# Performance work log

Hardware: AMD Instinct MI355X
Metric: run time of the kernel (lower is better)

Reference implementation:

```python
import jax, jax.numpy as jnp
import numpy as np

B, L, D = 1, 2048, 768
H, DH = 12, 64  # n_heads, d_head (D // H)
LN_EPS = 1e-5
DEN_EPS = 1e-6


def setup_inputs() -> dict:
    key = jax.random.key(0)
    ks = jax.random.split(key, 11)
    s = 0.02
    return {
        "x": jax.random.normal(ks[0], (B, L, D), dtype=jnp.float32),
        "W_qkv": jax.random.normal(ks[1], (D, 3 * D), dtype=jnp.float32) * s,
        "b_qkv": jnp.zeros((3 * D,), dtype=jnp.float32),
        "W_sem": jax.random.normal(ks[2], (D, 2 * D), dtype=jnp.float32) * s,
        "b_sem": jnp.zeros((2 * D,), dtype=jnp.float32),
        "W_ctx": jax.random.normal(ks[3], (D, 2 * D), dtype=jnp.float32) * s,
        "b_ctx": jnp.zeros((2 * D,), dtype=jnp.float32),
        "W_proj": jax.random.normal(ks[4], (D, D), dtype=jnp.float32) * s,
        "b_proj": jnp.zeros((D,), dtype=jnp.float32),
        "ln_g": jnp.ones((D,), dtype=jnp.float32),
        "ln_b": jnp.zeros((D,), dtype=jnp.float32),
    }


def _heads(t):
    # [B,L,D] -> [B,H,L,DH]
    return t.reshape(B, L, H, DH).transpose(0, 2, 1, 3)


def reference(x, W_qkv, b_qkv, W_sem, b_sem, W_ctx, b_ctx, W_proj, b_proj, ln_g, ln_b):
    # LayerNorm
    mu = jnp.mean(x, axis=-1, keepdims=True)
    var = jnp.mean(jnp.square(x - mu), axis=-1, keepdims=True)
    x_norm = (x - mu) * jax.lax.rsqrt(var + LN_EPS) * ln_g + ln_b

    qkv = x_norm @ W_qkv + b_qkv
    q, k, v = jnp.split(qkv, 3, axis=-1)

    # interference gate from raw x
    sem = x @ W_sem + b_sem
    sem_amp = jax.nn.softplus(sem[..., :D])
    sem_phase = sem[..., D:]
    ctx = x @ W_ctx + b_ctx
    ctx_amp = jax.nn.softplus(ctx[..., :D])
    ctx_phase = ctx[..., D:]
    gate = jax.nn.sigmoid(sem_amp * ctx_amp * jnp.cos(sem_phase - ctx_phase))
    k = k * gate

    q_f = jax.nn.elu(_heads(q)) + 1.0  # [B,H,L,DH]
    k_f = jax.nn.elu(_heads(k)) + 1.0
    v_f = _heads(v)

    # causal linear attention: cumsum of kv outer products along L
    kv = jnp.einsum("bhld,bhle->bhlde", k_f, v_f)  # [B,H,L,DH,DH]
    kv_cum = jnp.cumsum(kv, axis=2)
    out_num = jnp.einsum("bhld,bhlde->bhle", q_f, kv_cum)  # [B,H,L,DH]

    k_cum = jnp.cumsum(k_f, axis=2)
    out_den = jnp.sum(q_f * k_cum, axis=-1, keepdims=True) + DEN_EPS

    attn = (out_num / out_den).transpose(0, 2, 1, 3).reshape(B, L, D)
    return attn @ W_proj + b_proj
```

## Files before the change

kernel.cpp:

```cpp
#include <hip/hip_runtime.h>
#include <math.h>

#define LSEQ 2048
#define DMODEL 768
#define NHEAD 12
#define DHEAD 64
#define NCHUNK 32
#define NMERGED 5376

typedef unsigned short ushort_t;
typedef __attribute__((ext_vector_type(8))) short short8;
typedef float float4v __attribute__((ext_vector_type(4)));

__device__ __forceinline__ ushort_t f2b(float f) {
    union { float f; unsigned int u; } v; v.f = f;
    unsigned int u = v.u;
    return (ushort_t)((u + 0x7fffu + ((u >> 16) & 1u)) >> 16);
}
__device__ __forceinline__ float b2f(ushort_t u) {
    union { unsigned int u; float f; } v; v.u = ((unsigned int)u) << 16;
    return v.f;
}

__device__ __forceinline__ void gl_lds16(const ushort_t* g, ushort_t* l) {
    __builtin_amdgcn_global_load_lds(
        (const __attribute__((address_space(1))) unsigned int*)g,
        (__attribute__((address_space(3))) unsigned int*)l, 16, 0, 0);
}

__global__ void pre_kernel(const float* __restrict__ x, const float* __restrict__ g,
                           const float* __restrict__ beta, ushort_t* __restrict__ xn,
                           ushort_t* __restrict__ xb,
                           const float* __restrict__ Wq, const float* __restrict__ Ws,
                           const float* __restrict__ Wc, ushort_t* __restrict__ Tm,
                           const float* __restrict__ Wp, ushort_t* __restrict__ Tp) {
    __shared__ float red[4];
    __shared__ float bc;
    __shared__ float tile[32][33];
    int tid = threadIdx.x;
    if (blockIdx.x < 2048) {
        int row = blockIdx.x;
        const float* xr = x + (size_t)row * DMODEL;
        float v0 = xr[tid], v1 = xr[tid + 256], v2 = xr[tid + 512];
        float s = v0 + v1 + v2;
#pragma unroll
        for (int o = 32; o > 0; o >>= 1) s += __shfl_down(s, o);
        if ((tid & 63) == 0) red[tid >> 6] = s;
        __syncthreads();
        if (tid == 0) bc = (red[0] + red[1] + red[2] + red[3]) * (1.0f / DMODEL);
        __syncthreads();
        float mu = bc;
        float d0 = v0 - mu, d1 = v1 - mu, d2 = v2 - mu;
        float vs = d0 * d0 + d1 * d1 + d2 * d2;
        __syncthreads();
#pragma unroll
        for (int o = 32; o > 0; o >>= 1) vs += __shfl_down(vs, o);
        if ((tid & 63) == 0) red[tid >> 6] = vs;
        __syncthreads();
        if (tid == 0) bc = rsqrtf((red[0] + red[1] + red[2] + red[3]) * (1.0f / DMODEL) + 1e-5f);
        __syncthreads();
        float r = bc;
        ushort_t* xo = xn + (size_t)row * DMODEL;
        ushort_t* xc = xb + (size_t)row * DMODEL;
        xo[tid]       = f2b(d0 * r * g[tid]       + beta[tid]);
        xo[tid + 256] = f2b(d1 * r * g[tid + 256] + beta[tid + 256]);
        xo[tid + 512] = f2b(d2 * r * g[tid + 512] + beta[tid + 512]);
        xc[tid]       = f2b(v0);
        xc[tid + 256] = f2b(v1);
        xc[tid + 512] = f2b(v2);
    } else {
        int bid = blockIdx.x - 2048;
        int nb = bid % 72;
        int kb = (bid / 72) % 24;
        int zb = bid / (72 * 24);
        const float* W; ushort_t* Wt; int N;
        switch (zb) {
            case 0: W = Wq; Wt = Tm;                        N = 2304; break;
            case 1: W = Ws; Wt = Tm + (size_t)2304 * 768;   N = 1536; break;
            case 2: W = Wc; Wt = Tm + (size_t)3840 * 768;   N = 1536; break;
            default: W = Wp; Wt = Tp;                       N = 768;  break;
        }
        int nbase = nb * 32;
        if (nbase >= N) return;
        int tr = tid >> 5, tc = tid & 31;
        int kbase = kb * 32;
#pragma unroll
        for (int p = 0; p < 4; p++) {
            int r = p * 8 + tr;
            tile[r][tc] = W[(size_t)(kbase + r) * N + nbase + tc];
        }
        __syncthreads();
#pragma unroll
        for (int p = 0; p < 4; p++) {
            int r = p * 8 + tr;
            Wt[(size_t)(nbase + r) * 768 + kbase + tc] = f2b(tile[tc][r]);
        }
    }
}

__global__ __launch_bounds__(256) void gemm_merged_kernel(
    const ushort_t* __restrict__ Axn, const ushort_t* __restrict__ Axb,
    const ushort_t* __restrict__ Bt,
    const float* __restrict__ b_qkv, const float* __restrict__ b_sem,
    const float* __restrict__ b_ctx, ushort_t* __restrict__ Cb,
    ushort_t* __restrict__ vb) {
    const int K = 768;
    __shared__ ushort_t As[128 * 32];
    __shared__ ushort_t Bs[128 * 32];
    int tid = threadIdx.x;
    int wave = tid >> 6, lane = tid & 63;
    int wm = (wave >> 1) * 64, wn = (wave & 1) * 64;
    int quad = lane >> 4, l16 = lane & 15;
    int bid = blockIdx.x;
    int xcd = bid & 7, slot = bid >> 3;
    int tile_id = xcd * 84 + slot;
    int m0 = (tile_id & 15) * 128;
    int n0 = (tile_id >> 4) * 128;
    const ushort_t* A = (n0 < 2304) ? Axn : Axb;
    const float* bias = (n0 < 2304) ? (b_qkv + n0) : (n0 < 3840 ? (b_sem + n0 - 2304) : (b_ctx + n0 - 3840));

    int r0 = tid >> 2;
    int kc = (tid & 3) * 8;
    const ushort_t* Ag0 = A + (size_t)(m0 + r0) * K + kc;
    const ushort_t* Ag1 = A + (size_t)(m0 + 64 + r0) * K + kc;
    const ushort_t* Bg0 = Bt + (size_t)(n0 + r0) * K + kc;
    const ushort_t* Bg1 = Bt + (size_t)(n0 + 64 + r0) * K + kc;
    ushort_t* Al0 = &As[(wave * 64) * 8];
    ushort_t* Al1 = &As[(256 + wave * 64) * 8];
    ushort_t* Bl0 = &Bs[(wave * 64) * 8];
    ushort_t* Bl1 = &Bs[(256 + wave * 64) * 8];

    float4v acc[4][4];
#pragma unroll
    for (int i = 0; i < 4; i++)
#pragma unroll
        for (int j = 0; j < 4; j++)
#pragma unroll
            for (int r = 0; r < 4; r++) acc[i][j][r] = 0.0f;

    for (int k0 = 0; k0 < K; k0 += 32) {
        gl_lds16(Ag0 + k0, Al0);
        gl_lds16(Ag1 + k0, Al1);
        gl_lds16(Bg0 + k0, Bl0);
        gl_lds16(Bg1 + k0, Bl1);
        __syncthreads();
        short8 af[4], bf[4];
#pragma unroll
        for (int i = 0; i < 4; i++) af[i] = *(const short8*)&As[(wm + i * 16 + l16) * 32 + quad * 8];
#pragma unroll
        for (int j = 0; j < 4; j++) bf[j] = *(const short8*)&Bs[(wn + j * 16 + l16) * 32 + quad * 8];
#pragma unroll
        for (int i = 0; i < 4; i++)
#pragma unroll
            for (int j = 0; j < 4; j++)
                acc[i][j] = __builtin_amdgcn_mfma_f32_16x16x32_bf16(af[i], bf[j], acc[i][j], 0, 0, 0);
        __syncthreads();
    }
    bool is_v = (n0 >= 1536 && n0 < 2304);
#pragma unroll
    for (int i = 0; i < 4; i++) {
#pragma unroll
        for (int j = 0; j < 4; j++) {
            int colb = wn + j * 16 + l16;
            float bv = bias[colb];
#pragma unroll
            for (int r = 0; r < 4; r++) {
                int row = m0 + wm + i * 16 + quad * 4 + r;
                ushort_t o = f2b(acc[i][j][r] + bv);
                if (is_v) {
                    vb[(size_t)row * DMODEL + (n0 - 1536) + colb] = o;
                } else {
                    Cb[(size_t)row * NMERGED + n0 + colb] = o;
                }
            }
        }
    }
}

__global__ __launch_bounds__(256) void gemm_64_kernel(
    const ushort_t* __restrict__ A, const ushort_t* __restrict__ Bt,
    const float* __restrict__ bias, float* __restrict__ C,
    int N, int K) {
    __shared__ ushort_t As[64 * 32];
    __shared__ ushort_t Bs[64 * 32];
    int tid = threadIdx.x;
    int wave = tid >> 6, lane = tid & 63;
    int wm = (wave >> 1) * 32, wn = (wave & 1) * 32;
    int quad = lane >> 4, l16 = lane & 15;
    int m0 = blockIdx.y * 64, n0 = blockIdx.x * 64;

    int r0 = tid >> 2;
    int kc = (tid & 3) * 8;
    const ushort_t* Ag = A + (size_t)(m0 + r0) * K + kc;
    const ushort_t* Bg = Bt + (size_t)(n0 + r0) * K + kc;
    ushort_t* Al = &As[(wave * 16) * 32];
    ushort_t* Bl = &Bs[(wave * 16) * 32];

    float4v acc[2][2];
#pragma unroll
    for (int i = 0; i < 2; i++)
#pragma unroll
        for (int j = 0; j < 2; j++)
#pragma unroll
            for (int r = 0; r < 4; r++) acc[i][j][r] = 0.0f;

    for (int k0 = 0; k0 < K; k0 += 32) {
        gl_lds16(Ag + k0, Al);
        gl_lds16(Bg + k0, Bl);
        __syncthreads();
        short8 af[2], bf[2];
#pragma unroll
        for (int i = 0; i < 2; i++) af[i] = *(const short8*)&As[(wm + i * 16 + l16) * 32 + quad * 8];
#pragma unroll
        for (int j = 0; j < 2; j++) bf[j] = *(const short8*)&Bs[(wn + j * 16 + l16) * 32 + quad * 8];
#pragma unroll
        for (int i = 0; i < 2; i++)
#pragma unroll
            for (int j = 0; j < 2; j++)
                acc[i][j] = __builtin_amdgcn_mfma_f32_16x16x32_bf16(af[i], bf[j], acc[i][j], 0, 0, 0);
        __syncthreads();
    }
#pragma unroll
    for (int i = 0; i < 2; i++) {
#pragma unroll
        for (int j = 0; j < 2; j++) {
            int col = n0 + wn + j * 16 + l16;
            float bv = bias[col];
#pragma unroll
            for (int r = 0; r < 4; r++) {
                int row = m0 + wm + i * 16 + quad * 4 + r;
                C[(size_t)row * N + col] = acc[i][j][r] + bv;
            }
        }
    }
}

__device__ __forceinline__ float softplus_f(float x) {
    return (x > 15.f) ? x : log1pf(expf(x));
}

__global__ __launch_bounds__(256) void chunk_gate_mfma(const ushort_t* __restrict__ qscb,
                                                       const ushort_t* __restrict__ vb,
                                                       ushort_t* __restrict__ qf,
                                                       ushort_t* __restrict__ kf,
                                                       float* __restrict__ S) {
    int h = blockIdx.x % NHEAD;
    int c = blockIdx.x / NHEAD;
    __shared__ ushort_t Kt[64 * 72];
    __shared__ ushort_t Vt[64 * 72];
    int tid = threadIdx.x;
    const int hb = h * DHEAD;
#pragma unroll
    for (int it = 0; it < 4; it++) {
        int r = it * 16 + (tid >> 4);
        int cc = (tid & 15) * 4;
        int lg = c * 64 + r;
        size_t qb = (size_t)lg * NMERGED + hb + cc;
        ushort_t q4[4], k4[4], sa4[4], sp4[4], ca4[4], cp4[4], vt4[4];
        *(uint2*)q4  = *(const uint2*)&qscb[qb];
        *(uint2*)k4  = *(const uint2*)&qscb[qb + 768];
        *(uint2*)sa4 = *(const uint2*)&qscb[qb + 2304];
        *(uint2*)sp4 = *(const uint2*)&qscb[qb + 3072];
        *(uint2*)ca4 = *(const uint2*)&qscb[qb + 3840];
        *(uint2*)cp4 = *(const uint2*)&qscb[qb + 4608];
        *(uint2*)vt4 = *(const uint2*)&vb[(size_t)lg * DMODEL + hb + cc];
        ushort_t qo[4], ko[4];
#pragma unroll
        for (int i2 = 0; i2 < 4; i2++) {
            float amp = softplus_f(b2f(sa4[i2])) * softplus_f(b2f(ca4[i2]));
            float tt = amp * cosf(b2f(sp4[i2]) - b2f(cp4[i2]));
            float gate = 1.0f / (1.0f + expf(-tt));
            float kv = b2f(k4[i2]) * gate;
            float qv = b2f(q4[i2]);
            qo[i2] = f2b((qv > 0.f) ? qv + 1.0f : expf(qv));
            ko[i2] = f2b((kv > 0.f) ? kv + 1.0f : expf(kv));
            Kt[(cc + i2) * 72 + r] = ko[i2];
            Vt[(cc + i2) * 72 + r] = vt4[i2];
        }
        size_t o = (size_t)lg * DMODEL + hb + cc;
        *(uint2*)&qf[o] = *(uint2*)qo;
        *(uint2*)&kf[o] = *(uint2*)ko;
    }
    __syncthreads();
    int wave = tid >> 6, lane = tid & 63, quad = lane >> 4, l16 = lane & 15;
    int wm = wave * 16;
    float4v acc[4];
#pragma unroll
    for (int jt = 0; jt < 4; jt++)
#pragma unroll
        for (int r = 0; r < 4; r++) acc[jt][r] = 0.0f;
#pragma unroll
    for (int ks = 0; ks < 2; ks++) {
        short8 af = *(const short8*)&Kt[(wm + l16) * 72 + ks * 32 + quad * 8];
#pragma unroll
        for (int jt = 0; jt < 4; jt++) {
            short8 bf = *(const short8*)&Vt[(jt * 16 + l16) * 72 + ks * 32 + quad * 8];
            acc[jt] = __builtin_amdgcn_mfma_f32_16x16x32_bf16(af, bf, acc[jt], 0, 0, 0);
        }
    }
    float* Sp = S + (size_t)(h * NCHUNK + c) * 4160;
#pragma unroll
    for (int jt = 0; jt < 4; jt++) {
        float4 o;
        o.x = acc[jt][0]; o.y = acc[jt][1]; o.z = acc[jt][2]; o.w = acc[jt][3];
        *(float4*)&Sp[(jt * 16 + l16) * 64 + wm + quad * 4] = o;
    }
    if (tid < 64) {
        float s = 0.f;
#pragma unroll
        for (int g = 0; g < 8; g++) {
            short8 kv8 = *(const short8*)&Kt[tid * 72 + g * 8];
#pragma unroll
            for (int i2 = 0; i2 < 8; i2++) s += b2f(((ushort_t*)&kv8)[i2]);
        }
        Sp[4096 + tid] = s;
    }
}

__global__ void prefix_kernel(const float* __restrict__ S, ushort_t* __restrict__ Pb,
                              float* __restrict__ kpf) {
    int h = blockIdx.x;
    int i = blockIdx.y * 256 + threadIdx.x;
    if (i >= 4160) return;
    float v[NCHUNK];
    size_t base = (size_t)h * NCHUNK * 4160 + i;
#pragma unroll
    for (int c2 = 0; c2 < NCHUNK; c2++) v[c2] = S[base + (size_t)c2 * 4160];
    float run = 0.f;
    if (i < 4096) {
        size_t pb = (size_t)h * NCHUNK * 4096 + i;
#pragma unroll
        for (int c2 = 0; c2 < NCHUNK; c2++) {
            Pb[pb + (size_t)c2 * 4096] = f2b(run);
            run += v[c2];
        }
    } else {
        size_t kb = (size_t)h * NCHUNK * 64 + (i - 4096);
#pragma unroll
        for (int c2 = 0; c2 < NCHUNK; c2++) {
            kpf[kb + (size_t)c2 * 64] = run;
            run += v[c2];
        }
    }
}

__global__ __launch_bounds__(256) void attn_out_mfma(const ushort_t* __restrict__ qf,
                                                     const ushort_t* __restrict__ kf,
                                                     const ushort_t* __restrict__ vb,
                                                     const ushort_t* __restrict__ Pb,
                                                     const float* __restrict__ kpf,
                                                     ushort_t* __restrict__ attn) {
    int h = blockIdx.x % NHEAD;
    int c = blockIdx.x / NHEAD;
    __shared__ ushort_t Qs[64 * 72];
    __shared__ ushort_t Ks[64 * 72];
    __shared__ ushort_t Pt[64 * 72];
    __shared__ ushort_t Vt[64 * 72];
    __shared__ float Sc[64 * 68];
    __shared__ float kpl[64];
    __shared__ float denp[4][64];
    __shared__ float dnl[64];
    int tid = threadIdx.x;
    const size_t hb = (size_t)h * DHEAD;
    const size_t pcb = (size_t)(h * NCHUNK + c);
#pragma unroll
    for (int it = 0; it < 2; it++) {
        int chunk = it * 256 + tid;
        int r = chunk >> 3, c8 = (chunk & 7) * 8;
        int lg = c * 64 + r;
        *(uint4*)&Qs[r * 72 + c8] = *(const uint4*)&qf[(size_t)lg * DMODEL + hb + c8];
        *(uint4*)&Ks[r * 72 + c8] = *(const uint4*)&kf[(size_t)lg * DMODEL + hb + c8];
        *(uint4*)&Pt[r * 72 + c8] = *(const uint4*)&Pb[pcb * 4096 + r * 64 + c8];
    }
#pragma unroll
    for (int it = 0; it < 4; it++) {
        int r = it * 16 + (tid >> 4);
        int cc = (tid & 15) * 4;
        int lg = c * 64 + r;
        ushort_t vt4[4];
        *(uint2*)vt4 = *(const uint2*)&vb[(size_t)lg * DMODEL + hb + cc];
#pragma unroll
        for (int i2 = 0; i2 < 4; i2++) Vt[(cc + i2) * 72 + r] = vt4[i2];
    }
    if (tid < 64) kpl[tid] = kpf[pcb * 64 + tid];
    __syncthreads();
    int wave = tid >> 6, lane = tid & 63, quad = lane >> 4, l16 = lane & 15;
    int wm = wave * 16;
    float4v s_acc[4], n_acc[4];
#pragma unroll
    for (int jt = 0; jt < 4; jt++)
#pragma unroll
        for (int r = 0; r < 4; r++) { s_acc[jt][r] = 0.0f; n_acc[jt][r] = 0.0f; }
#pragma unroll
    for (int ks = 0; ks < 2; ks++) {
        short8 aq = *(const short8*)&Qs[(wm + l16) * 72 + ks * 32 + quad * 8];
#pragma unroll
        for (int jt = 0; jt < 4; jt++) {
            short8 bk = *(const short8*)&Ks[(jt * 16 + l16) * 72 + ks * 32 + quad * 8];
            short8 bp = *(const short8*)&Pt[(jt * 16 + l16) * 72 + ks * 32 + quad * 8];
            s_acc[jt] = __builtin_amdgcn_mfma_f32_16x16x32_bf16(aq, bk, s_acc[jt], 0, 0, 0);
            n_acc[jt] = __builtin_amdgcn_mfma_f32_16x16x32_bf16(aq, bp, n_acc[jt], 0, 0, 0);
        }
    }
#pragma unroll
    for (int jt = 0; jt < 4; jt++)
#pragma unroll
        for (int r = 0; r < 4; r++)
            Sc[(wm + quad * 4 + r) * 68 + jt * 16 + l16] = s_acc[jt][r];
    __syncthreads();
    {
        int l = tid & 63, part = tid >> 6;
        float s = 0.f;
#pragma unroll
        for (int jj = 0; jj < 16; jj++) {
            int j = part * 16 + jj;
            float v = Sc[l * 68 + j];
            s += (j <= l) ? v : 0.f;
        }
#pragma unroll
        for (int dd = 0; dd < 16; dd++) {
            int d = part * 16 + dd;
            s += b2f(Qs[l * 72 + d]) * kpl[d];
        }
        denp[part][l] = s;
    }
    __syncthreads();
    if (tid < 64) dnl[tid] = denp[0][tid] + denp[1][tid] + denp[2][tid] + denp[3][tid] + 1e-6f;
    __syncthreads();
#pragma unroll
    for (int ks = 0; ks < 2; ks++) {
        int m = wm + l16;
        float sv[8];
        *(float4*)&sv[0] = *(const float4*)&Sc[m * 68 + ks * 32 + quad * 8];
        *(float4*)&sv[4] = *(const float4*)&Sc[m * 68 + ks * 32 + quad * 8 + 4];
        ushort_t am[8];
#pragma unroll
        for (int i2 = 0; i2 < 8; i2++) {
            int j = ks * 32 + quad * 8 + i2;
            am[i2] = (j <= m) ? f2b(sv[i2]) : (ushort_t)0;
        }
        short8 af = *(short8*)am;
#pragma unroll
        for (int jt = 0; jt < 4; jt++) {
            short8 bv = *(const short8*)&Vt[(jt * 16 + l16) * 72 + ks * 32 + quad * 8];
            n_acc[jt] = __builtin_amdgcn_mfma_f32_16x16x32_bf16(af, bv, n_acc[jt], 0, 0, 0);
        }
    }
#pragma unroll
    for (int jt = 0; jt < 4; jt++) {
        int e = jt * 16 + l16;
#pragma unroll
        for (int r = 0; r < 4; r++) {
            int l = wm + quad * 4 + r;
            float o = n_acc[jt][r] / dnl[l];
            attn[(size_t)(c * 64 + l) * DMODEL + hb + e] = f2b(o);
        }
    }
}

extern "C" void kernel_launch(void* const* d_in, const int* in_sizes, int n_in,
                              void* d_out, int out_size, void* d_ws, size_t ws_size,
                              hipStream_t stream) {
    const float* x      = (const float*)d_in[0];
    const float* W_qkv  = (const float*)d_in[1];
    const float* b_qkv  = (const float*)d_in[2];
    const float* W_sem  = (const float*)d_in[3];
    const float* b_sem  = (const float*)d_in[4];
    const float* W_ctx  = (const float*)d_in[5];
    const float* b_ctx  = (const float*)d_in[6];
    const float* W_proj = (const float*)d_in[7];
    const float* b_proj = (const float*)d_in[8];
    const float* ln_g   = (const float*)d_in[9];
    const float* ln_b   = (const float*)d_in[10];
    float* out = (float*)d_out;
    float* ws  = (float*)d_ws;

    ushort_t* Wt_merged = (ushort_t*)(ws);
    ushort_t* Wt_proj   = (ushort_t*)(ws + 2064384);
    ushort_t* xb        = (ushort_t*)(ws + 2359296);
    ushort_t* xnb       = (ushort_t*)(ws + 3145728);
    ushort_t* qscb      = (ushort_t*)(ws + 3932160);
    ushort_t* vb        = (ushort_t*)(ws + 14942208);
    ushort_t* qf        = (ushort_t*)(ws + 2359296);
    ushort_t* kf        = (ushort_t*)(ws + 3145728);
    float*    S         = ws;
    ushort_t* Pb        = (ushort_t*)(ws + 3932160);
    float*    kpf       = ws + 4718592;
    ushort_t* attnb     = (ushort_t*)(ws);

    pre_kernel<<<2048 + 72 * 24 * 4, 256, 0, stream>>>(x, ln_g, ln_b, xnb, xb,
                                                       W_qkv, W_sem, W_ctx, Wt_merged,
                                                       W_proj, Wt_proj);

    gemm_merged_kernel<<<672, 256, 0, stream>>>(
        xnb, xb, Wt_merged, b_qkv, b_sem, b_ctx, qscb, vb);

    chunk_gate_mfma<<<NHEAD * NCHUNK, 256, 0, stream>>>(qscb, vb, qf, kf, S);
    prefix_kernel<<<dim3(NHEAD, 17), 256, 0, stream>>>(S, Pb, kpf);
    attn_out_mfma<<<NHEAD * NCHUNK, 256, 0, stream>>>(qf, kf, vb, Pb, kpf, attnb);

    gemm_64_kernel<<<dim3(768 / 64, LSEQ / 64), 256, 0, stream>>>(attnb, Wt_proj, b_proj, out, 768, 768);
}
```

Baseline: 165.7 us.

## Double-buffer and swizzle GEMM LDS tiles; compute q feature map in attention kernel

Both MFMA GEMM kernels now use two LDS buffers, so global-to-LDS loads for the next K-slice are issued before computing the current one. An XOR swizzle on the LDS column layout is meant to reduce bank conflicts on fragment reads. The elu+1 feature map for q moves from the gate kernel into the attention-output kernel, which reads q straight from the merged GEMM output and removes the qf intermediate buffer. The workspace offsets for Pb/kpf are relocated to avoid overlap with qscb, which is now still live. LDS usage doubles, which may reduce occupancy.

```diff
diff --git a/kernel.cpp b/kernel.cpp
--- a/kernel.cpp
+++ b/kernel.cpp
@@ -105,8 +105,8 @@
     const float* __restrict__ b_ctx, ushort_t* __restrict__ Cb,
     ushort_t* __restrict__ vb) {
     const int K = 768;
-    __shared__ ushort_t As[128 * 32];
-    __shared__ ushort_t Bs[128 * 32];
+    __shared__ ushort_t As[2][128 * 32];
+    __shared__ ushort_t Bs[2][128 * 32];
     int tid = threadIdx.x;
     int wave = tid >> 6, lane = tid & 63;
     int wm = (wave >> 1) * 64, wn = (wave & 1) * 64;
@@ -120,15 +120,13 @@
     const float* bias = (n0 < 2304) ? (b_qkv + n0) : (n0 < 3840 ? (b_sem + n0 - 2304) : (b_ctx + n0 - 3840));
 
     int r0 = tid >> 2;
-    int kc = (tid & 3) * 8;
+    int kc = ((tid & 3) ^ ((r0 >> 1) & 3)) * 8;
     const ushort_t* Ag0 = A + (size_t)(m0 + r0) * K + kc;
     const ushort_t* Ag1 = A + (size_t)(m0 + 64 + r0) * K + kc;
     const ushort_t* Bg0 = Bt + (size_t)(n0 + r0) * K + kc;
     const ushort_t* Bg1 = Bt + (size_t)(n0 + 64 + r0) * K + kc;
-    ushort_t* Al0 = &As[(wave * 64) * 8];
-    ushort_t* Al1 = &As[(256 + wave * 64) * 8];
-    ushort_t* Bl0 = &Bs[(wave * 64) * 8];
-    ushort_t* Bl1 = &Bs[(256 + wave * 64) * 8];
+    int ldsbase0 = (wave * 64) * 8;
+    int ldsbase1 = (256 + wave * 64) * 8;
 
     float4v acc[4][4];
 #pragma unroll
@@ -138,17 +136,32 @@
 #pragma unroll
             for (int r = 0; r < 4; r++) acc[i][j][r] = 0.0f;
 
-    for (int k0 = 0; k0 < K; k0 += 32) {
-        gl_lds16(Ag0 + k0, Al0);
-        gl_lds16(Ag1 + k0, Al1);
-        gl_lds16(Bg0 + k0, Bl0);
-        gl_lds16(Bg1 + k0, Bl1);
-        __syncthreads();
+    gl_lds16(Ag0, &As[0][ldsbase0]);
+    gl_lds16(Ag1, &As[0][ldsbase1]);
+    gl_lds16(Bg0, &Bs[0][ldsbase0]);
+    gl_lds16(Bg1, &Bs[0][ldsbase1]);
+    __syncthreads();
+    for (int it = 0; it < K / 32; it++) {
+        int cur = it & 1;
+        int k1 = (it + 1) * 32;
+        if (k1 < K) {
+            int nxt = cur ^ 1;
+            gl_lds16(Ag0 + k1, &As[nxt][ldsbase0]);
+            gl_lds16(Ag1 + k1, &As[nxt][ldsbase1]);
+            gl_lds16(Bg0 + k1, &Bs[nxt][ldsbase0]);
+            gl_lds16(Bg1 + k1, &Bs[nxt][ldsbase1]);
+        }
         short8 af[4], bf[4];
 #pragma unroll
-        for (int i = 0; i < 4; i++) af[i] = *(const short8*)&As[(wm + i * 16 + l16) * 32 + quad * 8];
-#pragma unroll
-        for (int j = 0; j < 4; j++) bf[j] = *(const short8*)&Bs[(wn + j * 16 + l16) * 32 + quad * 8];
+        for (int i = 0; i < 4; i++) {
+            int rr = wm + i * 16 + l16;
+            af[i] = *(const short8*)&As[cur][rr * 32 + ((quad ^ ((rr >> 1) & 3)) * 8)];
+        }
+#pragma unroll
+        for (int j = 0; j < 4; j++) {
+            int rr = wn + j * 16 + l16;
+            bf[j] = *(const short8*)&Bs[cur][rr * 32 + ((quad ^ ((rr >> 1) & 3)) * 8)];
+        }
 #pragma unroll
         for (int i = 0; i < 4; i++)
 #pragma unroll
@@ -181,8 +194,8 @@
     const ushort_t* __restrict__ A, const ushort_t* __restrict__ Bt,
     const float* __restrict__ bias, float* __restrict__ C,
     int N, int K) {
-    __shared__ ushort_t As[64 * 32];
-    __shared__ ushort_t Bs[64 * 32];
+    __shared__ ushort_t As[2][64 * 32];
+    __shared__ ushort_t Bs[2][64 * 32];
     int tid = threadIdx.x;
     int wave = tid >> 6, lane = tid & 63;
     int wm = (wave >> 1) * 32, wn = (wave & 1) * 32;
@@ -190,11 +203,10 @@
     int m0 = blockIdx.y * 64, n0 = blockIdx.x * 64;
 
     int r0 = tid >> 2;
-    int kc = (tid & 3) * 8;
+    int kc = ((tid & 3) ^ ((r0 >> 1) & 3)) * 8;
     const ushort_t* Ag = A + (size_t)(m0 + r0) * K + kc;
     const ushort_t* Bg = Bt + (size_t)(n0 + r0) * K + kc;
-    ushort_t* Al = &As[(wave * 16) * 32];
-    ushort_t* Bl = &Bs[(wave * 16) * 32];
+    int ldsbase = (wave * 64) * 8;
 
     float4v acc[2][2];
 #pragma unroll
@@ -204,15 +216,28 @@
 #pragma unroll
             for (int r = 0; r < 4; r++) acc[i][j][r] = 0.0f;
 
-    for (int k0 = 0; k0 < K; k0 += 32) {
-        gl_lds16(Ag + k0, Al);
-        gl_lds16(Bg + k0, Bl);
-        __syncthreads();
+    gl_lds16(Ag, &As[0][ldsbase]);
+    gl_lds16(Bg, &Bs[0][ldsbase]);
+    __syncthreads();
+    for (int it = 0; it < K / 32; it++) {
+        int cur = it & 1;
+        int k1 = (it + 1) * 32;
+        if (k1 < K) {
+            int nxt = cur ^ 1;
+            gl_lds16(Ag + k1, &As[nxt][ldsbase]);
+            gl_lds16(Bg + k1, &Bs[nxt][ldsbase]);
+        }
         short8 af[2], bf[2];
 #pragma unroll
-        for (int i = 0; i < 2; i++) af[i] = *(const short8*)&As[(wm + i * 16 + l16) * 32 + quad * 8];
-#pragma unroll
-        for (int j = 0; j < 2; j++) bf[j] = *(const short8*)&Bs[(wn + j * 16 + l16) * 32 + quad * 8];
+        for (int i = 0; i < 2; i++) {
+            int rr = wm + i * 16 + l16;
+            af[i] = *(const short8*)&As[cur][rr * 32 + ((quad ^ ((rr >> 1) & 3)) * 8)];
+        }
+#pragma unroll
+        for (int j = 0; j < 2; j++) {
+            int rr = wn + j * 16 + l16;
+            bf[j] = *(const short8*)&Bs[cur][rr * 32 + ((quad ^ ((rr >> 1) & 3)) * 8)];
+        }
 #pragma unroll
         for (int i = 0; i < 2; i++)
 #pragma unroll
@@ -239,11 +264,10 @@
     return (x > 15.f) ? x : log1pf(expf(x));
 }
 
-__global__ __launch_bounds__(256) void chunk_gate_mfma(const ushort_t* __restrict__ qscb,
-                                                       const ushort_t* __restrict__ vb,
-                                                       ushort_t* __restrict__ qf,
-                                                       ushort_t* __restrict__ kf,
-                                                       float* __restrict__ S) {
+__global__ __launch_bounds__(256) void chunk_kv_mfma(const ushort_t* __restrict__ qscb,
+                                                     const ushort_t* __restrict__ vb,
+                                                     ushort_t* __restrict__ kf,
+                                                     float* __restrict__ S) {
     int h = blockIdx.x % NHEAD;
     int c = blockIdx.x / NHEAD;
     __shared__ ushort_t Kt[64 * 72];
@@ -256,30 +280,25 @@
         int cc = (tid & 15) * 4;
         int lg = c * 64 + r;
         size_t qb = (size_t)lg * NMERGED + hb + cc;
-        ushort_t q4[4], k4[4], sa4[4], sp4[4], ca4[4], cp4[4], vt4[4];
-        *(uint2*)q4  = *(const uint2*)&qscb[qb];
+        ushort_t k4[4], sa4[4], sp4[4], ca4[4], cp4[4], vt4[4];
         *(uint2*)k4  = *(const uint2*)&qscb[qb + 768];
         *(uint2*)sa4 = *(const uint2*)&qscb[qb + 2304];
         *(uint2*)sp4 = *(const uint2*)&qscb[qb + 3072];
         *(uint2*)ca4 = *(const uint2*)&qscb[qb + 3840];
         *(uint2*)cp4 = *(const uint2*)&qscb[qb + 4608];
         *(uint2*)vt4 = *(const uint2*)&vb[(size_t)lg * DMODEL + hb + cc];
-        ushort_t qo[4], ko[4];
+        ushort_t ko[4];
 #pragma unroll
         for (int i2 = 0; i2 < 4; i2++) {
             float amp = softplus_f(b2f(sa4[i2])) * softplus_f(b2f(ca4[i2]));
             float tt = amp * cosf(b2f(sp4[i2]) - b2f(cp4[i2]));
             float gate = 1.0f / (1.0f + expf(-tt));
             float kv = b2f(k4[i2]) * gate;
-            float qv = b2f(q4[i2]);
-            qo[i2] = f2b((qv > 0.f) ? qv + 1.0f : expf(qv));
             ko[i2] = f2b((kv > 0.f) ? kv + 1.0f : expf(kv));
             Kt[(cc + i2) * 72 + r] = ko[i2];
             Vt[(cc + i2) * 72 + r] = vt4[i2];
         }
-        size_t o = (size_t)lg * DMODEL + hb + cc;
-        *(uint2*)&qf[o] = *(uint2*)qo;
-        *(uint2*)&kf[o] = *(uint2*)ko;
+        *(uint2*)&kf[(size_t)lg * DMODEL + hb + cc] = *(uint2*)ko;
     }
     __syncthreads();
     int wave = tid >> 6, lane = tid & 63, quad = lane >> 4, l16 = lane & 15;
@@ -344,7 +363,7 @@
     }
 }
 
-__global__ __launch_bounds__(256) void attn_out_mfma(const ushort_t* __restrict__ qf,
+__global__ __launch_bounds__(256) void attn_out_mfma(const ushort_t* __restrict__ qscb,
                                                      const ushort_t* __restrict__ kf,
                                                      const ushort_t* __restrict__ vb,
                                                      const ushort_t* __restrict__ Pb,
@@ -368,7 +387,14 @@
         int chunk = it * 256 + tid;
         int r = chunk >> 3, c8 = (chunk & 7) * 8;
         int lg = c * 64 + r;
-        *(uint4*)&Qs[r * 72 + c8] = *(const uint4*)&qf[(size_t)lg * DMODEL + hb + c8];
+        ushort_t q8[8], qo[8];
+        *(uint4*)q8 = *(const uint4*)&qscb[(size_t)lg * NMERGED + hb + c8];
+#pragma unroll
+        for (int i2 = 0; i2 < 8; i2++) {
+            float qv = b2f(q8[i2]);
+            qo[i2] = f2b((qv > 0.f) ? qv + 1.0f : expf(qv));
+        }
+        *(uint4*)&Qs[r * 72 + c8] = *(uint4*)qo;
         *(uint4*)&Ks[r * 72 + c8] = *(const uint4*)&kf[(size_t)lg * DMODEL + hb + c8];
         *(uint4*)&Pt[r * 72 + c8] = *(const uint4*)&Pb[pcb * 4096 + r * 64 + c8];
     }
@@ -481,11 +507,10 @@
     ushort_t* xnb       = (ushort_t*)(ws + 3145728);
     ushort_t* qscb      = (ushort_t*)(ws + 3932160);
     ushort_t* vb        = (ushort_t*)(ws + 14942208);
-    ushort_t* qf        = (ushort_t*)(ws + 2359296);
     ushort_t* kf        = (ushort_t*)(ws + 3145728);
     float*    S         = ws;
-    ushort_t* Pb        = (ushort_t*)(ws + 3932160);
-    float*    kpf       = ws + 4718592;
+    ushort_t* Pb        = (ushort_t*)(ws + 16777216);
+    float*    kpf       = ws + 17563648;
     ushort_t* attnb     = (ushort_t*)(ws);
 
     pre_kernel<<<2048 + 72 * 24 * 4, 256, 0, stream>>>(x, ln_g, ln_b, xnb, xb,
@@ -495,9 +520,9 @@
     gemm_merged_kernel<<<672, 256, 0, stream>>>(
         xnb, xb, Wt_merged, b_qkv, b_sem, b_ctx, qscb, vb);
 
-    chunk_gate_mfma<<<NHEAD * NCHUNK, 256, 0, stream>>>(qscb, vb, qf, kf, S);
+    chunk_kv_mfma<<<NHEAD * NCHUNK, 256, 0, stream>>>(qscb, vb, kf, S);
     prefix_kernel<<<dim3(NHEAD, 17), 256, 0, stream>>>(S, Pb, kpf);
-    attn_out_mfma<<<NHEAD * NCHUNK, 256, 0, stream>>>(qf, kf, vb, Pb, kpf, attnb);
+    attn_out_mfma<<<NHEAD * NCHUNK, 256, 0, stream>>>(qscb, kf, vb, Pb, kpf, attnb);
 
     gemm_64_kernel<<<dim3(768 / 64, LSEQ / 64), 256, 0, stream>>>(attnb, Wt_proj, b_proj, out, 768, 768);
 }
```

Measured after the change: 168.5 us. About the same (+1.6%).
